# Kernel optimization log

Hardware: AMD Instinct MI355X
Metric: run time of the kernel (lower is better)

## Reference

```python
import jax, jax.numpy as jnp
import numpy as np

KERNEL_SIZE = 5
EPS = 1e-4


def _sliding_sum(a, k, axis):
    cs = jnp.cumsum(a, axis=axis)
    zshape = list(a.shape)
    zshape[axis] = 1
    cs = jnp.concatenate([jnp.zeros(zshape, a.dtype), cs], axis=axis)
    n = cs.shape[axis]
    hi = jax.lax.slice_in_dim(cs, k, n, axis=axis)
    lo = jax.lax.slice_in_dim(cs, 0, n - k, axis=axis)
    return hi - lo


def box_blur(x, k):
    # x: [B, C, H, W]; normalized box filter with reflect padding (matches kornia box_blur)
    p = k // 2
    xp = jnp.pad(x, ((0, 0), (0, 0), (p, p), (p, p)), mode='reflect')
    s = _sliding_sum(_sliding_sum(xp, k, 2), k, 3)
    return s / jnp.asarray(k * k, x.dtype)


def guided_blur_multichannel(guidance, inp, k, eps):
    B, C, H, W = guidance.shape
    Cp = inp.shape[1]

    mean_I = box_blur(guidance, k)                                   # [B,C,H,W]
    corr_I = box_blur((guidance[:, None] * guidance[:, :, None]).reshape(B, C * C, H, W), k)
    var_I = corr_I.reshape(B, C, C, H, W) - mean_I[:, None] * mean_I[:, :, None]

    mean_p = box_blur(inp, k)                                        # [B,Cp,H,W]
    corr_Ip = box_blur((inp[:, None] * guidance[:, :, None]).reshape(B, C * Cp, H, W), k)
    cov_Ip = corr_Ip.reshape(B, C, Cp, H, W) - mean_p[:, None] * mean_I[:, :, None]

    eye = jnp.eye(C, dtype=guidance.dtype).reshape(1, C, C, 1, 1) * eps
    A = jnp.transpose(var_I + eye, (0, 3, 4, 1, 2))                  # [B,H,W,C,C]
    rhs = jnp.transpose(cov_Ip, (0, 3, 4, 1, 2))                     # [B,H,W,C,Cp]
    a = jnp.linalg.solve(A, rhs)                                     # [B,H,W,C,Cp]

    mean_I_hw = jnp.transpose(mean_I, (0, 2, 3, 1))                  # [B,H,W,C]
    mean_p_hw = jnp.transpose(mean_p, (0, 2, 3, 1))                  # [B,H,W,Cp]
    b = mean_p_hw - jnp.einsum('bhwcp,bhwc->bhwp', a, mean_I_hw)     # [B,H,W,Cp]

    a_ch = jnp.transpose(a.reshape(B, H, W, C * Cp), (0, 3, 1, 2))   # [B,C*Cp,H,W]
    b_ch = jnp.transpose(b, (0, 3, 1, 2))                            # [B,Cp,H,W]
    mean_a = jnp.transpose(box_blur(a_ch, k), (0, 2, 3, 1)).reshape(B, H, W, C, Cp)
    mean_b = box_blur(b_ch, k)                                       # [B,Cp,H,W]

    g_hw = jnp.transpose(guidance, (0, 2, 3, 1))                     # [B,H,W,C]
    out_hw = jnp.einsum('bhwc,bhwcp->bhwp', g_hw, mean_a)            # [B,H,W,Cp]
    return jnp.transpose(out_hw, (0, 3, 1, 2)) + mean_b              # [B,Cp,H,W]


def setup_inputs() -> dict:
    key = jax.random.key(0)
    k1, k2 = jax.random.split(key)
    guidance = jax.random.uniform(k1, (8, 3, 512, 512), dtype=jnp.float32)
    inp = jax.random.uniform(k2, (8, 3, 512, 512), dtype=jnp.float32)
    return {"guidance": guidance, "input": inp}


def reference(guidance, input):
    return guided_blur_multichannel(guidance, input, KERNEL_SIZE, EPS)
```

## Files before the change

kernel.cpp:

```cpp
#include <hip/hip_runtime.h>


namespace {

constexpr int BN = 8;
constexpr int HH = 512;
constexpr int WW = 512;
constexpr int CSZ = HH * WW;
constexpr float GEPS = 1e-4f;
constexpr int SEGW = 8;
constexpr int OUTW = 4 * SEGW;
constexpr int SR   = 32;

__device__ __forceinline__ int refl(int i, int n) {
    if (i < 0) i = -i;
    if (i >= n) i = 2 * n - 2 - i;
    return i;
}

template <int N>
__device__ __forceinline__ float shlN(float v) {
    return __builtin_bit_cast(float,
        __builtin_amdgcn_update_dpp(0, __builtin_bit_cast(int, v),
                                    0x100 + N, 0xF, 0xF, true));
}
__device__ __forceinline__ float hsum5(float v) {
    float t = v + shlN<1>(v);
    float q = t + shlN<2>(t);
    return q + shlN<4>(v);
}

struct St {
    float P[6];
    float V1[21];
    float r1[5][6];
    float V2[12];
    float r2[5][12];
};

struct Ctx {
    const float *g0, *g1, *g2, *p0, *p1, *p2;
    float *o0, *o1, *o2;
    int yb, xr, xs;
    bool wr;
};

template <int I>
__device__ __forceinline__ void row(St& st, const Ctx& cx, int rrb) {
    const int rr = rrb + I;

    float c0 = st.P[0], c1 = st.P[1], c2 = st.P[2];
    float c3 = st.P[3], c4 = st.P[4], c5 = st.P[5];

    {
        const int yn = refl(cx.yb - 4 + rr + 1, HH);
        const int offn = yn * WW + cx.xr;
        st.P[0] = cx.g0[offn]; st.P[1] = cx.g1[offn]; st.P[2] = cx.g2[offn];
        st.P[3] = cx.p0[offn]; st.P[4] = cx.p1[offn]; st.P[5] = cx.p2[offn];
    }

    st.V1[0] += c0; st.V1[1] += c1; st.V1[2] += c2;
    st.V1[3] += c3; st.V1[4] += c4; st.V1[5] += c5;
    st.V1[6]  += c0 * c0; st.V1[7]  += c0 * c1; st.V1[8]  += c0 * c2;
    st.V1[9]  += c1 * c1; st.V1[10] += c1 * c2; st.V1[11] += c2 * c2;
    st.V1[12] += c0 * c3; st.V1[13] += c0 * c4; st.V1[14] += c0 * c5;
    st.V1[15] += c1 * c3; st.V1[16] += c1 * c4; st.V1[17] += c1 * c5;
    st.V1[18] += c2 * c3; st.V1[19] += c2 * c4; st.V1[20] += c2 * c5;

    if (rr >= 5) {
        float o0 = st.r1[I][0], o1 = st.r1[I][1], o2 = st.r1[I][2];
        float o3 = st.r1[I][3], o4 = st.r1[I][4], o5 = st.r1[I][5];
        st.V1[0] -= o0; st.V1[1] -= o1; st.V1[2] -= o2;
        st.V1[3] -= o3; st.V1[4] -= o4; st.V1[5] -= o5;
        st.V1[6]  -= o0 * o0; st.V1[7]  -= o0 * o1; st.V1[8]  -= o0 * o2;
        st.V1[9]  -= o1 * o1; st.V1[10] -= o1 * o2; st.V1[11] -= o2 * o2;
        st.V1[12] -= o0 * o3; st.V1[13] -= o0 * o4; st.V1[14] -= o0 * o5;
        st.V1[15] -= o1 * o3; st.V1[16] -= o1 * o4; st.V1[17] -= o1 * o5;
        st.V1[18] -= o2 * o3; st.V1[19] -= o2 * o4; st.V1[20] -= o2 * o5;
    }
    st.r1[I][0] = c0; st.r1[I][1] = c1; st.r1[I][2] = c2;
    st.r1[I][3] = c3; st.r1[I][4] = c4; st.r1[I][5] = c5;

    if (rr >= 4) {
        float S[21];
#pragma unroll
        for (int c = 0; c < 21; ++c) S[c] = hsum5(st.V1[c]);

        const float nrm = 0.04f;
        float mI0 = S[0] * nrm, mI1 = S[1] * nrm, mI2 = S[2] * nrm;
        float mP0 = S[3] * nrm, mP1 = S[4] * nrm, mP2 = S[5] * nrm;
        float v00 = S[6]  * nrm - mI0 * mI0 + GEPS;
        float v01 = S[7]  * nrm - mI0 * mI1;
        float v02 = S[8]  * nrm - mI0 * mI2;
        float v11 = S[9]  * nrm - mI1 * mI1 + GEPS;
        float v12 = S[10] * nrm - mI1 * mI2;
        float v22 = S[11] * nrm - mI2 * mI2 + GEPS;
        float c00 = S[12] * nrm - mI0 * mP0;
        float c01 = S[13] * nrm - mI0 * mP1;
        float c02 = S[14] * nrm - mI0 * mP2;
        float c10 = S[15] * nrm - mI1 * mP0;
        float c11 = S[16] * nrm - mI1 * mP1;
        float c12 = S[17] * nrm - mI1 * mP2;
        float c20 = S[18] * nrm - mI2 * mP0;
        float c21 = S[19] * nrm - mI2 * mP1;
        float c22 = S[20] * nrm - mI2 * mP2;
        float i00 = v11 * v22 - v12 * v12;
        float i01 = v02 * v12 - v01 * v22;
        float i02 = v01 * v12 - v02 * v11;
        float i11 = v00 * v22 - v02 * v02;
        float i12 = v01 * v02 - v00 * v12;
        float i22 = v00 * v11 - v01 * v01;
        float det = v00 * i00 + v01 * i01 + v02 * i02;
        float rd  = __builtin_amdgcn_rcpf(det);
        float a00 = (i00 * c00 + i01 * c10 + i02 * c20) * rd;
        float a01 = (i00 * c01 + i01 * c11 + i02 * c21) * rd;
        float a02 = (i00 * c02 + i01 * c12 + i02 * c22) * rd;
        float a10 = (i01 * c00 + i11 * c10 + i12 * c20) * rd;
        float a11 = (i01 * c01 + i11 * c11 + i12 * c21) * rd;
        float a12 = (i01 * c02 + i11 * c12 + i12 * c22) * rd;
        float a20 = (i02 * c00 + i12 * c10 + i22 * c20) * rd;
        float a21 = (i02 * c01 + i12 * c11 + i22 * c21) * rd;
        float a22 = (i02 * c02 + i12 * c12 + i22 * c22) * rd;
        float b0 = mP0 - (a00 * mI0 + a10 * mI1 + a20 * mI2);
        float b1 = mP1 - (a01 * mI0 + a11 * mI1 + a21 * mI2);
        float b2 = mP2 - (a02 * mI0 + a12 * mI1 + a22 * mI2);

        float hv[12];
        hv[0] = hsum5(a00); hv[1]  = hsum5(a01); hv[2]  = hsum5(a02);
        hv[3] = hsum5(a10); hv[4]  = hsum5(a11); hv[5]  = hsum5(a12);
        hv[6] = hsum5(a20); hv[7]  = hsum5(a21); hv[8]  = hsum5(a22);
        hv[9] = hsum5(b0);  hv[10] = hsum5(b1);  hv[11] = hsum5(b2);

        if (rr >= 9) {
#pragma unroll
            for (int c = 0; c < 12; ++c) {
                st.V2[c] += hv[c] - st.r2[I][c];
                st.r2[I][c] = hv[c];
            }
        } else {
#pragma unroll
            for (int c = 0; c < 12; ++c) {
                st.V2[c] += hv[c];
                st.r2[I][c] = hv[c];
            }
        }

        if (rr >= 8) {
            constexpr int J = (I + 1) % 5;
            float gg0 = shlN<4>(st.r1[J][0]);
            float gg1 = shlN<4>(st.r1[J][1]);
            float gg2 = shlN<4>(st.r1[J][2]);
            const int oOff = (cx.yb + rr - 8) * WW + cx.xs;
            float M[12];
#pragma unroll
            for (int c = 0; c < 12; ++c) M[c] = st.V2[c] * 0.04f;
            float o0 = gg0 * M[0] + gg1 * M[3] + gg2 * M[6] + M[9];
            float o1 = gg0 * M[1] + gg1 * M[4] + gg2 * M[7] + M[10];
            float o2 = gg0 * M[2] + gg1 * M[5] + gg2 * M[8] + M[11];
            if (cx.wr) {
                cx.o0[oOff] = o0;
                cx.o1[oOff] = o1;
                cx.o2[oOff] = o2;
            }
        }
    }
}

__global__ __launch_bounds__(64, 2) void fused_kernel(
        const float* __restrict__ g, const float* __restrict__ p,
        float* __restrict__ out) {
    const int lane = threadIdx.x;
    const int l    = lane & 15;
    const int seg  = lane >> 4;
    const int XO   = blockIdx.x * OUTW;
    const int bb   = blockIdx.z;

    const int xbase = XO + seg * SEGW - 2;
    const int xrq   = xbase + l - 2;
    const int xo    = xbase + l + 2;

    Ctx cx;
    cx.g0 = g + (size_t)bb * 3 * CSZ; cx.g1 = cx.g0 + CSZ; cx.g2 = cx.g0 + 2 * CSZ;
    cx.p0 = p + (size_t)bb * 3 * CSZ; cx.p1 = cx.p0 + CSZ; cx.p2 = cx.p0 + 2 * CSZ;
    cx.o0 = out + (size_t)bb * 3 * CSZ; cx.o1 = cx.o0 + CSZ; cx.o2 = cx.o0 + 2 * CSZ;
    cx.yb = blockIdx.y * SR;
    cx.xr = refl(xrq, WW);
    cx.xs = (xo < WW) ? xo : (WW - 1);
    cx.wr = (l < SEGW);

    St st;
#pragma unroll
    for (int i = 0; i < 21; ++i) st.V1[i] = 0.f;
#pragma unroll
    for (int i = 0; i < 12; ++i) st.V2[i] = 0.f;

    {
        const int y0 = refl(cx.yb - 4, HH);
        const int off0 = y0 * WW + cx.xr;
        st.P[0] = cx.g0[off0]; st.P[1] = cx.g1[off0]; st.P[2] = cx.g2[off0];
        st.P[3] = cx.p0[off0]; st.P[4] = cx.p1[off0]; st.P[5] = cx.p2[off0];
    }

#pragma unroll 1
    for (int t = 0; t < 8; ++t) {
        int rrb = 5 * t;
        asm("" : "+s"(rrb));
        row<0>(st, cx, rrb);
        row<1>(st, cx, rrb);
        row<2>(st, cx, rrb);
        row<3>(st, cx, rrb);
        row<4>(st, cx, rrb);
    }
}

}

extern "C" void kernel_launch(void* const* d_in, const int* in_sizes, int n_in,
                              void* d_out, int out_size, void* d_ws, size_t ws_size,
                              hipStream_t stream) {
    const float* g  = (const float*)d_in[0];
    const float* p  = (const float*)d_in[1];
    float* out = (float*)d_out;

    dim3 grid(WW / OUTW, HH / SR, BN);
    dim3 block(64);

    hipLaunchKernelGGL(fused_kernel, grid, block, 0, stream, g, p, out);
}
```

Measured before the change: 136.6 us.

## Process two pixels per lane, reload evicted rows, and peel row pipeline stages

Result: slower. 152.4 us (+11.5%).

```diff
diff --git a/kernel.cpp b/kernel.cpp
--- a/kernel.cpp
+++ b/kernel.cpp
@@ -8,9 +8,8 @@
 constexpr int WW = 512;
 constexpr int CSZ = HH * WW;
 constexpr float GEPS = 1e-4f;
-constexpr int SEGW = 8;
-constexpr int OUTW = 4 * SEGW;
-constexpr int SR   = 32;
+constexpr int OUTW = 96;
+constexpr int SR   = 16;
 
 __device__ __forceinline__ int refl(int i, int n) {
     if (i < 0) i = -i;
@@ -24,144 +23,162 @@
         __builtin_amdgcn_update_dpp(0, __builtin_bit_cast(int, v),
                                     0x100 + N, 0xF, 0xF, true));
 }
-__device__ __forceinline__ float hsum5(float v) {
-    float t = v + shlN<1>(v);
-    float q = t + shlN<2>(t);
-    return q + shlN<4>(v);
-}
 
 struct St {
-    float P[6];
-    float V1[21];
-    float r1[5][6];
-    float V2[12];
-    float r2[5][12];
+    float P[12];
+    float V1[2][21];
+    float r2[5][2][12];
 };
 
 struct Ctx {
     const float *g0, *g1, *g2, *p0, *p1, *p2;
     float *o0, *o1, *o2;
-    int yb, xr, xs;
-    bool wr;
+    int yb, xr0, xr1, xsE, xsO;
+    bool wrE, wrO;
 };
 
-template <int I>
-__device__ __forceinline__ void row(St& st, const Ctx& cx, int rrb) {
-    const int rr = rrb + I;
-
-    float c0 = st.P[0], c1 = st.P[1], c2 = st.P[2];
-    float c3 = st.P[3], c4 = st.P[4], c5 = st.P[5];
-
-    {
+__device__ __forceinline__ void solveS(const float (&S)[21], float (&A)[12]) {
+    const float nrm = 0.04f;
+    float mI0 = S[0] * nrm, mI1 = S[1] * nrm, mI2 = S[2] * nrm;
+    float mP0 = S[3] * nrm, mP1 = S[4] * nrm, mP2 = S[5] * nrm;
+    float v00 = S[6]  * nrm - mI0 * mI0 + GEPS;
+    float v01 = S[7]  * nrm - mI0 * mI1;
+    float v02 = S[8]  * nrm - mI0 * mI2;
+    float v11 = S[9]  * nrm - mI1 * mI1 + GEPS;
+    float v12 = S[10] * nrm - mI1 * mI2;
+    float v22 = S[11] * nrm - mI2 * mI2 + GEPS;
+    float c00 = S[12] * nrm - mI0 * mP0;
+    float c01 = S[13] * nrm - mI0 * mP1;
+    float c02 = S[14] * nrm - mI0 * mP2;
+    float c10 = S[15] * nrm - mI1 * mP0;
+    float c11 = S[16] * nrm - mI1 * mP1;
+    float c12 = S[17] * nrm - mI1 * mP2;
+    float c20 = S[18] * nrm - mI2 * mP0;
+    float c21 = S[19] * nrm - mI2 * mP1;
+    float c22 = S[20] * nrm - mI2 * mP2;
+    float i00 = v11 * v22 - v12 * v12;
+    float i01 = v02 * v12 - v01 * v22;
+    float i02 = v01 * v12 - v02 * v11;
+    float i11 = v00 * v22 - v02 * v02;
+    float i12 = v01 * v02 - v00 * v12;
+    float i22 = v00 * v11 - v01 * v01;
+    float det = v00 * i00 + v01 * i01 + v02 * i02;
+    float rd  = __builtin_amdgcn_rcpf(det);
+    float rs  = rd * 0.04f;
+    A[0] = (i00 * c00 + i01 * c10 + i02 * c20) * rs;
+    A[1] = (i00 * c01 + i01 * c11 + i02 * c21) * rs;
+    A[2] = (i00 * c02 + i01 * c12 + i02 * c22) * rs;
+    A[3] = (i01 * c00 + i11 * c10 + i12 * c20) * rs;
+    A[4] = (i01 * c01 + i11 * c11 + i12 * c21) * rs;
+    A[5] = (i01 * c02 + i11 * c12 + i12 * c22) * rs;
+    A[6] = (i02 * c00 + i12 * c10 + i22 * c20) * rs;
+    A[7] = (i02 * c01 + i12 * c11 + i22 * c21) * rs;
+    A[8] = (i02 * c02 + i12 * c12 + i22 * c22) * rs;
+    A[9]  = mP0 * 0.04f - (A[0] * mI0 + A[3] * mI1 + A[6] * mI2);
+    A[10] = mP1 * 0.04f - (A[1] * mI0 + A[4] * mI1 + A[7] * mI2);
+    A[11] = mP2 * 0.04f - (A[2] * mI0 + A[5] * mI1 + A[8] * mI2);
+}
+
+template <int PX>
+__device__ __forceinline__ void addStats(St& st, float c0, float c1, float c2,
+                                         float c3, float c4, float c5) {
+    st.V1[PX][0] += c0; st.V1[PX][1] += c1; st.V1[PX][2] += c2;
+    st.V1[PX][3] += c3; st.V1[PX][4] += c4; st.V1[PX][5] += c5;
+    st.V1[PX][6]  += c0 * c0; st.V1[PX][7]  += c0 * c1; st.V1[PX][8]  += c0 * c2;
+    st.V1[PX][9]  += c1 * c1; st.V1[PX][10] += c1 * c2; st.V1[PX][11] += c2 * c2;
+    st.V1[PX][12] += c0 * c3; st.V1[PX][13] += c0 * c4; st.V1[PX][14] += c0 * c5;
+    st.V1[PX][15] += c1 * c3; st.V1[PX][16] += c1 * c4; st.V1[PX][17] += c1 * c5;
+    st.V1[PX][18] += c2 * c3; st.V1[PX][19] += c2 * c4; st.V1[PX][20] += c2 * c5;
+}
+
+template <int PX>
+__device__ __forceinline__ void subStats(St& st, float c0, float c1, float c2,
+                                         float c3, float c4, float c5) {
+    st.V1[PX][0] -= c0; st.V1[PX][1] -= c1; st.V1[PX][2] -= c2;
+    st.V1[PX][3] -= c3; st.V1[PX][4] -= c4; st.V1[PX][5] -= c5;
+    st.V1[PX][6]  -= c0 * c0; st.V1[PX][7]  -= c0 * c1; st.V1[PX][8]  -= c0 * c2;
+    st.V1[PX][9]  -= c1 * c1; st.V1[PX][10] -= c1 * c2; st.V1[PX][11] -= c2 * c2;
+    st.V1[PX][12] -= c0 * c3; st.V1[PX][13] -= c0 * c4; st.V1[PX][14] -= c0 * c5;
+    st.V1[PX][15] -= c1 * c3; st.V1[PX][16] -= c1 * c4; st.V1[PX][17] -= c1 * c5;
+    st.V1[PX][18] -= c2 * c3; st.V1[PX][19] -= c2 * c4; st.V1[PX][20] -= c2 * c5;
+}
+
+template <int I, bool SUB1, bool SOLVE, bool OUT, bool PF>
+__device__ __forceinline__ void row(St& st, const Ctx& cx, int t) {
+    const int rr = 5 * t + I;
+
+    float c00 = st.P[0], c01 = st.P[1], c02 = st.P[2];
+    float c03 = st.P[3], c04 = st.P[4], c05 = st.P[5];
+    float c10 = st.P[6], c11 = st.P[7], c12 = st.P[8];
+    float c13 = st.P[9], c14 = st.P[10], c15 = st.P[11];
+
+    if constexpr (PF) {
         const int yn = refl(cx.yb - 4 + rr + 1, HH);
-        const int offn = yn * WW + cx.xr;
-        st.P[0] = cx.g0[offn]; st.P[1] = cx.g1[offn]; st.P[2] = cx.g2[offn];
-        st.P[3] = cx.p0[offn]; st.P[4] = cx.p1[offn]; st.P[5] = cx.p2[offn];
-    }
-
-    st.V1[0] += c0; st.V1[1] += c1; st.V1[2] += c2;
-    st.V1[3] += c3; st.V1[4] += c4; st.V1[5] += c5;
-    st.V1[6]  += c0 * c0; st.V1[7]  += c0 * c1; st.V1[8]  += c0 * c2;
-    st.V1[9]  += c1 * c1; st.V1[10] += c1 * c2; st.V1[11] += c2 * c2;
-    st.V1[12] += c0 * c3; st.V1[13] += c0 * c4; st.V1[14] += c0 * c5;
-    st.V1[15] += c1 * c3; st.V1[16] += c1 * c4; st.V1[17] += c1 * c5;
-    st.V1[18] += c2 * c3; st.V1[19] += c2 * c4; st.V1[20] += c2 * c5;
-
-    if (rr >= 5) {
-        float o0 = st.r1[I][0], o1 = st.r1[I][1], o2 = st.r1[I][2];
-        float o3 = st.r1[I][3], o4 = st.r1[I][4], o5 = st.r1[I][5];
-        st.V1[0] -= o0; st.V1[1] -= o1; st.V1[2] -= o2;
-        st.V1[3] -= o3; st.V1[4] -= o4; st.V1[5] -= o5;
-        st.V1[6]  -= o0 * o0; st.V1[7]  -= o0 * o1; st.V1[8]  -= o0 * o2;
-        st.V1[9]  -= o1 * o1; st.V1[10] -= o1 * o2; st.V1[11] -= o2 * o2;
-        st.V1[12] -= o0 * o3; st.V1[13] -= o0 * o4; st.V1[14] -= o0 * o5;
-        st.V1[15] -= o1 * o3; st.V1[16] -= o1 * o4; st.V1[17] -= o1 * o5;
-        st.V1[18] -= o2 * o3; st.V1[19] -= o2 * o4; st.V1[20] -= o2 * o5;
-    }
-    st.r1[I][0] = c0; st.r1[I][1] = c1; st.r1[I][2] = c2;
-    st.r1[I][3] = c3; st.r1[I][4] = c4; st.r1[I][5] = c5;
-
-    if (rr >= 4) {
-        float S[21];
-#pragma unroll
-        for (int c = 0; c < 21; ++c) S[c] = hsum5(st.V1[c]);
-
-        const float nrm = 0.04f;
-        float mI0 = S[0] * nrm, mI1 = S[1] * nrm, mI2 = S[2] * nrm;
-        float mP0 = S[3] * nrm, mP1 = S[4] * nrm, mP2 = S[5] * nrm;
-        float v00 = S[6]  * nrm - mI0 * mI0 + GEPS;
-        float v01 = S[7]  * nrm - mI0 * mI1;
-        float v02 = S[8]  * nrm - mI0 * mI2;
-        float v11 = S[9]  * nrm - mI1 * mI1 + GEPS;
-        float v12 = S[10] * nrm - mI1 * mI2;
-        float v22 = S[11] * nrm - mI2 * mI2 + GEPS;
-        float c00 = S[12] * nrm - mI0 * mP0;
-        float c01 = S[13] * nrm - mI0 * mP1;
-        float c02 = S[14] * nrm - mI0 * mP2;
-        float c10 = S[15] * nrm - mI1 * mP0;
-        float c11 = S[16] * nrm - mI1 * mP1;
-        float c12 = S[17] * nrm - mI1 * mP2;
-        float c20 = S[18] * nrm - mI2 * mP0;
-        float c21 = S[19] * nrm - mI2 * mP1;
-        float c22 = S[20] * nrm - mI2 * mP2;
-        float i00 = v11 * v22 - v12 * v12;
-        float i01 = v02 * v12 - v01 * v22;
-        float i02 = v01 * v12 - v02 * v11;
-        float i11 = v00 * v22 - v02 * v02;
-        float i12 = v01 * v02 - v00 * v12;
-        float i22 = v00 * v11 - v01 * v01;
-        float det = v00 * i00 + v01 * i01 + v02 * i02;
-        float rd  = __builtin_amdgcn_rcpf(det);
-        float a00 = (i00 * c00 + i01 * c10 + i02 * c20) * rd;
-        float a01 = (i00 * c01 + i01 * c11 + i02 * c21) * rd;
-        float a02 = (i00 * c02 + i01 * c12 + i02 * c22) * rd;
-        float a10 = (i01 * c00 + i11 * c10 + i12 * c20) * rd;
-        float a11 = (i01 * c01 + i11 * c11 + i12 * c21) * rd;
-        float a12 = (i01 * c02 + i11 * c12 + i12 * c22) * rd;
-        float a20 = (i02 * c00 + i12 * c10 + i22 * c20) * rd;
-        float a21 = (i02 * c01 + i12 * c11 + i22 * c21) * rd;
-        float a22 = (i02 * c02 + i12 * c12 + i22 * c22) * rd;
-        float b0 = mP0 - (a00 * mI0 + a10 * mI1 + a20 * mI2);
-        float b1 = mP1 - (a01 * mI0 + a11 * mI1 + a21 * mI2);
-        float b2 = mP2 - (a02 * mI0 + a12 * mI1 + a22 * mI2);
-
-        float hv[12];
-        hv[0] = hsum5(a00); hv[1]  = hsum5(a01); hv[2]  = hsum5(a02);
-        hv[3] = hsum5(a10); hv[4]  = hsum5(a11); hv[5]  = hsum5(a12);
-        hv[6] = hsum5(a20); hv[7]  = hsum5(a21); hv[8]  = hsum5(a22);
-        hv[9] = hsum5(b0);  hv[10] = hsum5(b1);  hv[11] = hsum5(b2);
-
-        if (rr >= 9) {
+        const int o0 = yn * WW + cx.xr0, o1 = yn * WW + cx.xr1;
+        st.P[0] = cx.g0[o0]; st.P[1]  = cx.g1[o0]; st.P[2]  = cx.g2[o0];
+        st.P[3] = cx.p0[o0]; st.P[4]  = cx.p1[o0]; st.P[5]  = cx.p2[o0];
+        st.P[6] = cx.g0[o1]; st.P[7]  = cx.g1[o1]; st.P[8]  = cx.g2[o1];
+        st.P[9] = cx.p0[o1]; st.P[10] = cx.p1[o1]; st.P[11] = cx.p2[o1];
+    }
+
+    if constexpr (SUB1) {
+        const int yo = refl(cx.yb + rr - 9, HH);
+        const int u0 = yo * WW + cx.xr0, u1 = yo * WW + cx.xr1;
+        float o00 = cx.g0[u0], o01 = cx.g1[u0], o02 = cx.g2[u0];
+        float o03 = cx.p0[u0], o04 = cx.p1[u0], o05 = cx.p2[u0];
+        float o10 = cx.g0[u1], o11 = cx.g1[u1], o12 = cx.g2[u1];
+        float o13 = cx.p0[u1], o14 = cx.p1[u1], o15 = cx.p2[u1];
+        subStats<0>(st, o00, o01, o02, o03, o04, o05);
+        subStats<1>(st, o10, o11, o12, o13, o14, o15);
+    }
+    addStats<0>(st, c00, c01, c02, c03, c04, c05);
+    addStats<1>(st, c10, c11, c12, c13, c14, c15);
+
+    if constexpr (SOLVE) {
+        float SE[21], SO[21];
+#pragma unroll
+        for (int c = 0; c < 21; ++c) {
+            float tt = shlN<1>(st.V1[0][c]) + st.V1[1][c];
+            float m  = tt + shlN<1>(tt);
+            SE[c] = st.V1[0][c] + m;
+            SO[c] = m + shlN<2>(st.V1[1][c]);
+        }
+        float A0[12], A1[12];
+        solveS(SE, A0);
+        solveS(SO, A1);
+
+#pragma unroll
+        for (int c = 0; c < 12; ++c) {
+            float tt = shlN<1>(A0[c]) + A1[c];
+            float m  = tt + shlN<1>(tt);
+            st.r2[I][0][c] = A0[c] + m;
+            st.r2[I][1][c] = m + shlN<2>(A1[c]);
+        }
+
+        if constexpr (OUT) {
+            constexpr int J1 = (I + 1) % 5, J2 = (I + 2) % 5;
+            constexpr int J3 = (I + 3) % 5, J4 = (I + 4) % 5;
+            float ME[12], MO[12];
 #pragma unroll
             for (int c = 0; c < 12; ++c) {
-                st.V2[c] += hv[c] - st.r2[I][c];
-                st.r2[I][c] = hv[c];
+                ME[c] = ((st.r2[I][0][c] + st.r2[J1][0][c]) +
+                         (st.r2[J2][0][c] + st.r2[J3][0][c])) + st.r2[J4][0][c];
+                MO[c] = ((st.r2[I][1][c] + st.r2[J1][1][c]) +
+                         (st.r2[J2][1][c] + st.r2[J3][1][c])) + st.r2[J4][1][c];
             }
-        } else {
-#pragma unroll
-            for (int c = 0; c < 12; ++c) {
-                st.V2[c] += hv[c];
-                st.r2[I][c] = hv[c];
-            }
-        }
-
-        if (rr >= 8) {
-            constexpr int J = (I + 1) % 5;
-            float gg0 = shlN<4>(st.r1[J][0]);
-            float gg1 = shlN<4>(st.r1[J][1]);
-            float gg2 = shlN<4>(st.r1[J][2]);
-            const int oOff = (cx.yb + rr - 8) * WW + cx.xs;
-            float M[12];
-#pragma unroll
-            for (int c = 0; c < 12; ++c) M[c] = st.V2[c] * 0.04f;
-            float o0 = gg0 * M[0] + gg1 * M[3] + gg2 * M[6] + M[9];
-            float o1 = gg0 * M[1] + gg1 * M[4] + gg2 * M[7] + M[10];
-            float o2 = gg0 * M[2] + gg1 * M[5] + gg2 * M[8] + M[11];
-            if (cx.wr) {
-                cx.o0[oOff] = o0;
-                cx.o1[oOff] = o1;
-                cx.o2[oOff] = o2;
-            }
+            const int yg = cx.yb + rr - 8;
+            const int q0 = yg * WW + cx.xr0, q1 = yg * WW + cx.xr1;
+            float gE0 = shlN<2>(cx.g0[q0]), gE1 = shlN<2>(cx.g1[q0]), gE2 = shlN<2>(cx.g2[q0]);
+            float gO0 = shlN<2>(cx.g0[q1]), gO1 = shlN<2>(cx.g1[q1]), gO2 = shlN<2>(cx.g2[q1]);
+            const int oE = yg * WW + cx.xsE, oO = yg * WW + cx.xsO;
+            float e0 = gE0 * ME[0] + gE1 * ME[3] + gE2 * ME[6] + ME[9];
+            float e1 = gE0 * ME[1] + gE1 * ME[4] + gE2 * ME[7] + ME[10];
+            float e2 = gE0 * ME[2] + gE1 * ME[5] + gE2 * ME[8] + ME[11];
+            float f0 = gO0 * MO[0] + gO1 * MO[3] + gO2 * MO[6] + MO[9];
+            float f1 = gO0 * MO[1] + gO1 * MO[4] + gO2 * MO[7] + MO[10];
+            float f2 = gO0 * MO[2] + gO1 * MO[5] + gO2 * MO[8] + MO[11];
+            if (cx.wrE) { cx.o0[oE] = e0; cx.o1[oE] = e1; cx.o2[oE] = e2; }
+            if (cx.wrO) { cx.o0[oO] = f0; cx.o1[oO] = f1; cx.o2[oO] = f2; }
         }
     }
 }
@@ -170,47 +187,65 @@
         const float* __restrict__ g, const float* __restrict__ p,
         float* __restrict__ out) {
     const int lane = threadIdx.x;
-    const int l    = lane & 15;
+    const int u    = lane & 15;
     const int seg  = lane >> 4;
     const int XO   = blockIdx.x * OUTW;
     const int bb   = blockIdx.z;
 
-    const int xbase = XO + seg * SEGW - 2;
-    const int xrq   = xbase + l - 2;
-    const int xo    = xbase + l + 2;
+    const int Ob  = XO + 24 * seg;
+    const int x0q = Ob + 2 * u - 4;
+    const int xoE = Ob + 2 * u;
+    const int xoO = xoE + 1;
 
     Ctx cx;
     cx.g0 = g + (size_t)bb * 3 * CSZ; cx.g1 = cx.g0 + CSZ; cx.g2 = cx.g0 + 2 * CSZ;
     cx.p0 = p + (size_t)bb * 3 * CSZ; cx.p1 = cx.p0 + CSZ; cx.p2 = cx.p0 + 2 * CSZ;
     cx.o0 = out + (size_t)bb * 3 * CSZ; cx.o1 = cx.o0 + CSZ; cx.o2 = cx.o0 + 2 * CSZ;
-    cx.yb = blockIdx.y * SR;
-    cx.xr = refl(xrq, WW);
-    cx.xs = (xo < WW) ? xo : (WW - 1);
-    cx.wr = (l < SEGW);
+    cx.yb  = blockIdx.y * SR;
+    cx.xr0 = refl(x0q, WW);
+    cx.xr1 = refl(x0q + 1, WW);
+    cx.xsE = (xoE < WW) ? xoE : (WW - 1);
+    cx.xsO = (xoO < WW) ? xoO : (WW - 1);
+    cx.wrE = (u < 12) && (xoE < WW);
+    cx.wrO = (u < 12) && (xoO < WW);
 
     St st;
 #pragma unroll
-    for (int i = 0; i < 21; ++i) st.V1[i] = 0.f;
-#pragma unroll
-    for (int i = 0; i < 12; ++i) st.V2[i] = 0.f;
+    for (int x = 0; x < 2; ++x)
+#pragma unroll
+        for (int i = 0; i < 21; ++i) st.V1[x][i] = 0.f;
 
     {
         const int y0 = refl(cx.yb - 4, HH);
-        const int off0 = y0 * WW + cx.xr;
-        st.P[0] = cx.g0[off0]; st.P[1] = cx.g1[off0]; st.P[2] = cx.g2[off0];
-        st.P[3] = cx.p0[off0]; st.P[4] = cx.p1[off0]; st.P[5] = cx.p2[off0];
-    }
-
+        const int a0 = y0 * WW + cx.xr0, a1 = y0 * WW + cx.xr1;
+        st.P[0] = cx.g0[a0]; st.P[1]  = cx.g1[a0]; st.P[2]  = cx.g2[a0];
+        st.P[3] = cx.p0[a0]; st.P[4]  = cx.p1[a0]; st.P[5]  = cx.p2[a0];
+        st.P[6] = cx.g0[a1]; st.P[7]  = cx.g1[a1]; st.P[8]  = cx.g2[a1];
+        st.P[9] = cx.p0[a1]; st.P[10] = cx.p1[a1]; st.P[11] = cx.p2[a1];
+    }
+
+    row<0, false, false, false, true>(st, cx, 0);
+    row<1, false, false, false, true>(st, cx, 0);
+    row<2, false, false, false, true>(st, cx, 0);
+    row<3, false, false, false, true>(st, cx, 0);
+    row<4, false, true,  false, true>(st, cx, 0);
+    row<0, true, true, false, true>(st, cx, 1);
+    row<1, true, true, false, true>(st, cx, 1);
+    row<2, true, true, false, true>(st, cx, 1);
+    row<3, true, true, true,  true>(st, cx, 1);
+    row<4, true, true, true,  true>(st, cx, 1);
 #pragma unroll 1
-    for (int t = 0; t < 8; ++t) {
-        int rrb = 5 * t;
-        asm("" : "+s"(rrb));
-        row<0>(st, cx, rrb);
-        row<1>(st, cx, rrb);
-        row<2>(st, cx, rrb);
-        row<3>(st, cx, rrb);
-        row<4>(st, cx, rrb);
-    }
+    for (int t = 2; t <= 3; ++t) {
+        row<0, true, true, true, true>(st, cx, t);
+        row<1, true, true, true, true>(st, cx, t);
+        row<2, true, true, true, true>(st, cx, t);
+        row<3, true, true, true, true>(st, cx, t);
+        row<4, true, true, true, true>(st, cx, t);
+    }
+    row<0, true, true, true, true >(st, cx, 4);
+    row<1, true, true, true, true >(st, cx, 4);
+    row<2, true, true, true, true >(st, cx, 4);
+    row<3, true, true, true, false>(st, cx, 4);
 }
 
 }
@@ -222,7 +257,7 @@
     const float* p  = (const float*)d_in[1];
     float* out = (float*)d_out;
 
-    dim3 grid(WW / OUTW, HH / SR, BN);
+    dim3 grid((WW + OUTW - 1) / OUTW, HH / SR, BN);
     dim3 block(64);
 
     hipLaunchKernelGGL(fused_kernel, grid, block, 0, stream, g, p, out);
```
